# Performance work log

Hardware: AMD Instinct MI355X
Metric: run time of the kernel (lower is better)

Reference implementation:

```python
import jax, jax.numpy as jnp
import numpy as np

D_MODEL = 1024

def setup_inputs() -> dict:
    key = jax.random.key(0)
    k1, k2, k3, k4, k5 = jax.random.split(key, 5)
    x = jax.random.normal(k1, (4, 2048, D_MODEL), dtype=jnp.float32)
    # torch nn.Linear weights: [out_features, in_features]
    W_qkv = jax.random.normal(k2, (3 * D_MODEL, D_MODEL), dtype=jnp.float32) * (1.0 / np.sqrt(D_MODEL))
    b_qkv = jax.random.normal(k3, (3 * D_MODEL,), dtype=jnp.float32) * 0.01
    W_proj = jax.random.normal(k4, (D_MODEL, D_MODEL), dtype=jnp.float32) * (1.0 / np.sqrt(D_MODEL))
    b_proj = jax.random.normal(k5, (D_MODEL,), dtype=jnp.float32) * 0.01
    return {"x": x, "W_qkv": W_qkv, "b_qkv": b_qkv, "W_proj": W_proj, "b_proj": b_proj}

def reference(x, W_qkv, b_qkv, W_proj, b_proj):
    # qkv projection: x @ W.T + b  (torch Linear convention)
    qkv = jnp.einsum('bsd,ed->bse', x, W_qkv) + b_qkv  # [B,S,3D]
    q, k, v = jnp.split(qkv, 3, axis=-1)               # each [B,S,D]
    scale = 1.0 / jnp.sqrt(jnp.asarray(q.shape[-1], dtype=q.dtype))
    scores = jnp.einsum('bqd,bkd->bqk', q, k) * scale   # [B,S,S]
    attn = jax.nn.softmax(scores, axis=-1)
    out = jnp.einsum('bqk,bkd->bqd', attn, v)           # [B,S,D]
    return jnp.einsum('bsd,ed->bse', out, W_proj) + b_proj
```

## Files before the change

kernel.cpp:

```cpp
#include <hip/hip_runtime.h>
#include <stdint.h>
#include <stddef.h>


typedef __attribute__((ext_vector_type(8))) short bf16x8;
typedef __attribute__((ext_vector_type(4))) float f32x4;

__device__ __forceinline__ unsigned short f2bf(float f) {
  unsigned u = __float_as_uint(f);
  u += 0x7fffu + ((u >> 16) & 1u);
  return (unsigned short)(u >> 16);
}
__device__ __forceinline__ float bf2f(unsigned short h) {
  return __uint_as_float(((unsigned)h) << 16);
}

typedef const __attribute__((address_space(1))) void* gas_ptr;
typedef __attribute__((address_space(3))) void* las_ptr;

__device__ __forceinline__ void gload_lds16(const void* g, void* l) {
  __builtin_amdgcn_global_load_lds((gas_ptr)(uintptr_t)g,
                                   (las_ptr)(uint32_t)(uintptr_t)l, 16, 0, 0);
}

__device__ __forceinline__ f32x4 mfma16(bf16x8 a, bf16x8 b, f32x4 c) {
  return __builtin_amdgcn_mfma_f32_16x16x32_bf16(a, b, c, 0, 0, 0);
}

__global__ __launch_bounds__(256) void cvt_f32_bf16(
    const float* __restrict__ in, unsigned short* __restrict__ out, int n) {
  int i = (blockIdx.x * blockDim.x + threadIdx.x) * 4;
  int stride = gridDim.x * blockDim.x * 4;
  for (; i < n; i += stride) {
    float4 v = *reinterpret_cast<const float4*>(in + i);
    ushort4 o;
    o.x = f2bf(v.x); o.y = f2bf(v.y); o.z = f2bf(v.z); o.w = f2bf(v.w);
    *reinterpret_cast<ushort4*>(out + i) = o;
  }
}

__device__ __forceinline__ void stage_gf(const unsigned short* __restrict__ P,
                                         int ld, unsigned short* dst, int wid,
                                         int lane) {
#pragma unroll
  for (int c = 0; c < 4; ++c) {
    int s = (c * 4 + wid) * 64 + lane;
    int row = s >> 3, g = s & 7;
    gload_lds16(P + (size_t)row * ld + ((g ^ (row & 7)) * 8),
                dst + (c * 4 + wid) * 512);
  }
}

template <bool OUT_BF16, bool HAS_BIAS, bool EXPOUT, bool TRANSOUT, bool RINV>
__global__ __launch_bounds__(256, 2) void gf(
    const unsigned short* __restrict__ A, const unsigned short* __restrict__ B,
    void* __restrict__ Cv, const float* __restrict__ bias,
    int K, int lda, int ldb, int ldc,
    long long strideA, long long strideB, long long strideC, float alpha) {
  __shared__ unsigned short lds[2][2][128 * 64];

  const int bz = blockIdx.z;
  const int gx = gridDim.x;
  int lin = blockIdx.y * gx + blockIdx.x;
  int bx, by;
  {
    const int nwg = gx * gridDim.y;
    const int q = nwg >> 3;
    lin = (lin & 7) * q + (lin >> 3);
    const int t = lin >> 6, r = lin & 63;
    const int tilesX = gx >> 3;
    bx = (t % tilesX) * 8 + (r & 7);
    by = (t / tilesX) * 8 + (r >> 3);
  }
  const int rowBase = by * 128;
  const int colBase = bx * 128;

  const unsigned short* Ap = A + (size_t)bz * (size_t)strideA + (size_t)rowBase * lda;
  const unsigned short* Bp = B + (size_t)bz * (size_t)strideB + (size_t)colBase * ldb;

  const int tid = threadIdx.x;
  const int wid = tid >> 6;
  const int lane = tid & 63;
  const int wr = wid >> 1;
  const int wc = wid & 1;
  const int fr = lane & 15;
  const int kgi = lane >> 4;

  const int nt = K >> 6;

  f32x4 acc[4][4] = {};
  f32x4 rsacc[4] = {};
  bf16x8 ones;
#pragma unroll
  for (int i = 0; i < 8; ++i) ones[i] = (short)0x3F80;

  stage_gf(Ap, lda, &lds[0][0][0], wid, lane);
  stage_gf(Bp, ldb, &lds[0][1][0], wid, lane);
  asm volatile("s_waitcnt vmcnt(0)" ::: "memory");
  __builtin_amdgcn_sched_barrier(0);
  __builtin_amdgcn_s_barrier();

  for (int t = 0; t < nt; ++t) {
    const int cur = t & 1;
    if (t + 1 < nt) {
      stage_gf(Ap + (size_t)(t + 1) * 64, lda, &lds[cur ^ 1][0][0], wid, lane);
      stage_gf(Bp + (size_t)(t + 1) * 64, ldb, &lds[cur ^ 1][1][0], wid, lane);
    }
    const unsigned short* sAc = &lds[cur][0][0];
    const unsigned short* sBc = &lds[cur][1][0];

    bf16x8 af[4][2], bv[4][2];
#pragma unroll
    for (int m = 0; m < 4; ++m) {
      int row = wr * 64 + m * 16 + fr;
      int r7 = row & 7;
      af[m][0] = *(const bf16x8*)&sAc[row * 64 + ((kgi ^ r7) * 8)];
      af[m][1] = *(const bf16x8*)&sAc[row * 64 + (((4 + kgi) ^ r7) * 8)];
    }
#pragma unroll
    for (int n = 0; n < 4; ++n) {
      int row = wc * 64 + n * 16 + fr;
      int r7 = row & 7;
      bv[n][0] = *(const bf16x8*)&sBc[row * 64 + ((kgi ^ r7) * 8)];
      bv[n][1] = *(const bf16x8*)&sBc[row * 64 + (((4 + kgi) ^ r7) * 8)];
    }
    asm volatile("s_waitcnt lgkmcnt(0)" ::: "memory");
    __builtin_amdgcn_sched_barrier(0);
    __builtin_amdgcn_s_setprio(1);
#pragma unroll
    for (int m = 0; m < 4; ++m)
#pragma unroll
      for (int n = 0; n < 4; ++n) {
        acc[m][n] = mfma16(af[m][0], bv[n][0], acc[m][n]);
        acc[m][n] = mfma16(af[m][1], bv[n][1], acc[m][n]);
      }
    if (RINV) {
#pragma unroll
      for (int m = 0; m < 4; ++m) {
        rsacc[m] = mfma16(af[m][0], ones, rsacc[m]);
        rsacc[m] = mfma16(af[m][1], ones, rsacc[m]);
      }
    }
    __builtin_amdgcn_s_setprio(0);
    __builtin_amdgcn_sched_barrier(0);
    asm volatile("s_waitcnt vmcnt(0)" ::: "memory");
    __builtin_amdgcn_sched_barrier(0);
    __builtin_amdgcn_s_barrier();
  }

  const int rg = (lane >> 4) * 4;

  if (TRANSOUT) {
    unsigned short* cl = &lds[0][0][0];
#pragma unroll
    for (int m = 0; m < 4; ++m) {
      int rloc0 = wr * 64 + m * 16 + rg;
#pragma unroll
      for (int n = 0; n < 4; ++n) {
        int cloc = wc * 64 + n * 16 + fr;
        float bvs = HAS_BIAS ? bias[colBase + cloc] : 0.0f;
#pragma unroll
        for (int j = 0; j < 4; ++j) {
          float v = acc[m][n][j] * alpha + bvs;
          cl[cloc * 136 + rloc0 + j] = f2bf(v);
        }
      }
    }
    __syncthreads();
    const int b = rowBase >> 11;
    const int s0 = rowBase & 2047;
    unsigned short* Vt = reinterpret_cast<unsigned short*>(Cv);
#pragma unroll
    for (int i = 0; i < 8; ++i) {
      int slot = i * 256 + tid;
      int d = slot >> 4, sg = slot & 15;
      bf16x8 v = *(const bf16x8*)&cl[d * 136 + sg * 8];
      *(bf16x8*)&Vt[((size_t)(b * 1024 + colBase + d)) * 2048 + s0 + sg * 8] = v;
    }
  } else if (OUT_BF16) {
    unsigned short* cl = &lds[0][0][0];
#pragma unroll
    for (int m = 0; m < 4; ++m) {
      int rloc0 = wr * 64 + m * 16 + rg;
      float rs4[4];
      if (RINV) {
#pragma unroll
        for (int j = 0; j < 4; ++j) rs4[j] = 1.0f / rsacc[m][j];
      }
#pragma unroll
      for (int n = 0; n < 4; ++n) {
        int cloc = wc * 64 + n * 16 + fr;
        float bvs = 0.0f;
        if (HAS_BIAS) bvs = bias[colBase + cloc];
#pragma unroll
        for (int j = 0; j < 4; ++j) {
          int row = rloc0 + j;
          float v = acc[m][n][j] * alpha;
          if (EXPOUT) v = __expf(v);
          else v += bvs;
          if (RINV) v *= rs4[j];
          int gW = cloc >> 3;
          int gS = (gW & 8) | ((gW & 7) ^ (row & 7));
          cl[row * 128 + gS * 8 + (cloc & 7)] = f2bf(v);
        }
      }
    }
    __syncthreads();
    unsigned short* Cb =
        reinterpret_cast<unsigned short*>(Cv) + (size_t)bz * (size_t)strideC;
#pragma unroll
    for (int i = 0; i < 8; ++i) {
      int slot = i * 256 + tid;
      int row = slot >> 4, g = slot & 15;
      int gS = (g & 8) | ((g & 7) ^ (row & 7));
      bf16x8 v = *(const bf16x8*)&cl[row * 128 + gS * 8];
      *(bf16x8*)&Cb[(size_t)(rowBase + row) * ldc + colBase + g * 8] = v;
    }
  } else {
    float* clf = reinterpret_cast<float*>(&lds[0][0][0]);
#pragma unroll
    for (int m = 0; m < 4; ++m) {
      int rloc0 = wr * 64 + m * 16 + rg;
#pragma unroll
      for (int n = 0; n < 4; ++n) {
        int cloc = wc * 64 + n * 16 + fr;
        float bvs = 0.0f;
        if (HAS_BIAS) bvs = bias[colBase + cloc];
#pragma unroll
        for (int j = 0; j < 4; ++j) {
          int row = rloc0 + j;
          float v = acc[m][n][j] * alpha + bvs;
          int gW = cloc >> 2;
          int gS = (gW & 24) | ((gW & 7) ^ (row & 7));
          clf[row * 128 + gS * 4 + (cloc & 3)] = v;
        }
      }
    }
    __syncthreads();
    float* Cf = reinterpret_cast<float*>(Cv) + (size_t)bz * (size_t)strideC;
#pragma unroll
    for (int i = 0; i < 16; ++i) {
      int slot = i * 256 + tid;
      int row = slot >> 5, g = slot & 31;
      int gS = (g & 24) | ((g & 7) ^ (row & 7));
      float4 v = *(const float4*)&clf[row * 128 + gS * 4];
      *(float4*)&Cf[(size_t)(rowBase + row) * ldc + colBase + g * 4] = v;
    }
  }
}

extern "C" void kernel_launch(void* const* d_in, const int* in_sizes, int n_in,
                              void* d_out, int out_size, void* d_ws, size_t ws_size,
                              hipStream_t stream) {
  const float* x     = (const float*)d_in[0];
  const float* Wqkv  = (const float*)d_in[1];
  const float* bqkv  = (const float*)d_in[2];
  const float* Wproj = (const float*)d_in[3];
  const float* bproj = (const float*)d_in[4];
  float* out = (float*)d_out;

  char* ws = (char*)d_ws;
  unsigned short* qk   = (unsigned short*)(ws + 0);
  unsigned short* xatt = (unsigned short*)(ws + 50331648);
  unsigned short* wq   = (unsigned short*)(ws + 67108864);
  unsigned short* wp   = (unsigned short*)(ws + 73400320);
  unsigned short* vt   = (unsigned short*)(ws + 75497472);
  unsigned short* sc   = (unsigned short*)(ws + 92274688);

  dim3 blk256(256);

  cvt_f32_bf16<<<2048, blk256, 0, stream>>>(x, xatt, 8192 * 1024);
  cvt_f32_bf16<<<1024, blk256, 0, stream>>>(Wqkv, wq, 3072 * 1024);
  cvt_f32_bf16<<<512, blk256, 0, stream>>>(Wproj, wp, 1024 * 1024);

  gf<true, true, false, false, false><<<dim3(16, 64, 1), blk256, 0, stream>>>(
      xatt, wq, qk, bqkv,
      1024, 1024, 1024, 2048, 0, 0, 0, 1.0f);

  gf<true, true, false, true, false><<<dim3(8, 64, 1), blk256, 0, stream>>>(
      xatt, wq + 2048 * 1024, vt, bqkv + 2048,
      1024, 1024, 1024, 2048, 0, 0, 0, 1.0f);

  gf<true, false, true, false, false><<<dim3(16, 16, 4), blk256, 0, stream>>>(
      qk, qk + 1024, sc, nullptr,
      1024, 2048, 2048, 2048,
      2048LL * 2048, 2048LL * 2048, 2048LL * 2048, 0.03125f);

  gf<true, false, false, false, true><<<dim3(8, 16, 4), blk256, 0, stream>>>(
      sc, vt, xatt, nullptr,
      2048, 2048, 2048, 1024,
      2048LL * 2048, 1024LL * 2048, 2048LL * 1024, 1.0f);

  gf<false, true, false, false, false><<<dim3(8, 64, 1), blk256, 0, stream>>>(
      xatt, wp, out, bproj,
      1024, 1024, 1024, 1024, 0, 0, 0, 1.0f);
}
```

Measured before the change: 176.6 us.

## Use 4-stage K=32 LDS pipeline with partial vmcnt waits in GEMM

Changes the GEMM main loop from a double-buffered K=64 tile to a 4-buffer ring of K=32 tiles, prefetching three stages ahead. It waits with partial vmcnt counts instead of draining all loads each iteration, and uses a new XOR swizzle matched to 32-wide rows. The aim is to hide global-load latency better. In exchange it runs twice as many iterations and barriers per K, drops the setprio hints, and relies on exact vmcnt accounting.

Measured after the change: 204.9 us. +16.0%, slower.

```diff
diff --git a/kernel.cpp b/kernel.cpp
--- a/kernel.cpp
+++ b/kernel.cpp
@@ -39,15 +39,16 @@
   }
 }
 
-__device__ __forceinline__ void stage_gf(const unsigned short* __restrict__ P,
-                                         int ld, unsigned short* dst, int wid,
-                                         int lane) {
-#pragma unroll
-  for (int c = 0; c < 4; ++c) {
-    int s = (c * 4 + wid) * 64 + lane;
-    int row = s >> 3, g = s & 7;
-    gload_lds16(P + (size_t)row * ld + ((g ^ (row & 7)) * 8),
-                dst + (c * 4 + wid) * 512);
+
+__device__ __forceinline__ void stage32(const unsigned short* __restrict__ P,
+                                        int ld, unsigned short* dst, int tid) {
+  const int w = tid >> 6, l = tid & 63;
+  const int rr = l >> 2;
+  const int cswz = (((l & 3) ^ ((l >> 3) & 3)) * 8);
+#pragma unroll
+  for (int c = 0; c < 2; ++c) {
+    int r = c * 64 + w * 16 + rr;
+    gload_lds16(P + (size_t)r * ld + cswz, dst + c * 2048 + w * 512);
   }
 }
 
@@ -57,7 +58,7 @@
     void* __restrict__ Cv, const float* __restrict__ bias,
     int K, int lda, int ldb, int ldc,
     long long strideA, long long strideB, long long strideC, float alpha) {
-  __shared__ unsigned short lds[2][2][128 * 64];
+  __shared__ unsigned short lds[4][2][128 * 32];
 
   const int bz = blockIdx.z;
   const int gx = gridDim.x;
@@ -85,8 +86,9 @@
   const int wc = wid & 1;
   const int fr = lane & 15;
   const int kgi = lane >> 4;
-
-  const int nt = K >> 6;
+  const int rcol = ((kgi ^ ((fr >> 1) & 3)) * 8);
+
+  const int nt = K >> 5;
 
   f32x4 acc[4][4] = {};
   f32x4 rsacc[4] = {};
@@ -94,59 +96,49 @@
 #pragma unroll
   for (int i = 0; i < 8; ++i) ones[i] = (short)0x3F80;
 
-  stage_gf(Ap, lda, &lds[0][0][0], wid, lane);
-  stage_gf(Bp, ldb, &lds[0][1][0], wid, lane);
-  asm volatile("s_waitcnt vmcnt(0)" ::: "memory");
-  __builtin_amdgcn_sched_barrier(0);
-  __builtin_amdgcn_s_barrier();
+#pragma unroll
+  for (int p = 0; p < 3; ++p) {
+    stage32(Ap + (size_t)p * 32, lda, &lds[p][0][0], tid);
+    stage32(Bp + (size_t)p * 32, ldb, &lds[p][1][0], tid);
+  }
 
   for (int t = 0; t < nt; ++t) {
-    const int cur = t & 1;
-    if (t + 1 < nt) {
-      stage_gf(Ap + (size_t)(t + 1) * 64, lda, &lds[cur ^ 1][0][0], wid, lane);
-      stage_gf(Bp + (size_t)(t + 1) * 64, ldb, &lds[cur ^ 1][1][0], wid, lane);
-    }
-    const unsigned short* sAc = &lds[cur][0][0];
-    const unsigned short* sBc = &lds[cur][1][0];
-
-    bf16x8 af[4][2], bv[4][2];
-#pragma unroll
-    for (int m = 0; m < 4; ++m) {
-      int row = wr * 64 + m * 16 + fr;
-      int r7 = row & 7;
-      af[m][0] = *(const bf16x8*)&sAc[row * 64 + ((kgi ^ r7) * 8)];
-      af[m][1] = *(const bf16x8*)&sAc[row * 64 + (((4 + kgi) ^ r7) * 8)];
-    }
-#pragma unroll
-    for (int n = 0; n < 4; ++n) {
-      int row = wc * 64 + n * 16 + fr;
-      int r7 = row & 7;
-      bv[n][0] = *(const bf16x8*)&sBc[row * 64 + ((kgi ^ r7) * 8)];
-      bv[n][1] = *(const bf16x8*)&sBc[row * 64 + (((4 + kgi) ^ r7) * 8)];
-    }
-    asm volatile("s_waitcnt lgkmcnt(0)" ::: "memory");
+    if (t + 2 < nt) {
+      asm volatile("s_waitcnt vmcnt(8)" ::: "memory");
+    } else if (t + 1 < nt) {
+      asm volatile("s_waitcnt vmcnt(4)" ::: "memory");
+    } else {
+      asm volatile("s_waitcnt vmcnt(0)" ::: "memory");
+    }
+    __builtin_amdgcn_s_barrier();
+
+    if (t + 3 < nt) {
+      stage32(Ap + (size_t)(t + 3) * 32, lda, &lds[(t + 3) & 3][0][0], tid);
+      stage32(Bp + (size_t)(t + 3) * 32, ldb, &lds[(t + 3) & 3][1][0], tid);
+    }
+
+    const unsigned short* sAc = &lds[t & 3][0][0];
+    const unsigned short* sBc = &lds[t & 3][1][0];
+    bf16x8 af[4], bv[4];
+#pragma unroll
+    for (int m = 0; m < 4; ++m)
+      af[m] = *(const bf16x8*)&sAc[(wr * 64 + m * 16 + fr) * 32 + rcol];
+#pragma unroll
+    for (int n = 0; n < 4; ++n)
+      bv[n] = *(const bf16x8*)&sBc[(wc * 64 + n * 16 + fr) * 32 + rcol];
+#pragma unroll
+    for (int m = 0; m < 4; ++m)
+#pragma unroll
+      for (int n = 0; n < 4; ++n)
+        acc[m][n] = mfma16(af[m], bv[n], acc[m][n]);
+    if (RINV) {
+#pragma unroll
+      for (int m = 0; m < 4; ++m) rsacc[m] = mfma16(af[m], ones, rsacc[m]);
+    }
     __builtin_amdgcn_sched_barrier(0);
-    __builtin_amdgcn_s_setprio(1);
-#pragma unroll
-    for (int m = 0; m < 4; ++m)
-#pragma unroll
-      for (int n = 0; n < 4; ++n) {
-        acc[m][n] = mfma16(af[m][0], bv[n][0], acc[m][n]);
-        acc[m][n] = mfma16(af[m][1], bv[n][1], acc[m][n]);
-      }
-    if (RINV) {
-#pragma unroll
-      for (int m = 0; m < 4; ++m) {
-        rsacc[m] = mfma16(af[m][0], ones, rsacc[m]);
-        rsacc[m] = mfma16(af[m][1], ones, rsacc[m]);
-      }
-    }
-    __builtin_amdgcn_s_setprio(0);
-    __builtin_amdgcn_sched_barrier(0);
-    asm volatile("s_waitcnt vmcnt(0)" ::: "memory");
-    __builtin_amdgcn_sched_barrier(0);
-    __builtin_amdgcn_s_barrier();
-  }
+  }
+
+  __syncthreads();
 
   const int rg = (lane >> 4) * 4;
 
```
